# Performance work log

Measured on AMD Instinct MI355X. Metric: run time of the kernel, lower is better.

The kernel has to match this reference:

```python
import jax, jax.numpy as jnp
import numpy as np

# HEALPix face halo padding following the DLWP-HPX / HEALPixPad scheme:
# 12 faces (0-3 north polar, 4-7 equatorial, 8-11 south polar), each face
# padded with rotated/flipped slabs of its neighbor faces; missing tri-point
# corners of equatorial faces are synthesized from the two adjacent edges.

def _rot(f, k):
    # rotate a face [B, C, H, W] in its spatial plane
    return jnp.rot90(f, k, axes=(-2, -1))

def _corner_tl(top, left, p):
    # Missing top-left corner (tri-point): mean of the two adjacent pixels,
    # remaining halo pixels copied from the adjoining edges.
    ret = jnp.zeros(top.shape[:-2] + (p, p), top.dtype)
    ret = ret.at[..., -1, -1].set(0.5 * (top[..., -1, 0] + left[..., 0, -1]))
    for i in range(1, p):
        ret = ret.at[..., -i - 1, -1].set(top[..., -i - 1, 0])
        ret = ret.at[..., -1, -i - 1].set(left[..., 0, -i - 1])
    return ret

def _corner_br(bottom, right, p):
    # Missing bottom-right corner (tri-point)
    ret = jnp.zeros(bottom.shape[:-2] + (p, p), bottom.dtype)
    ret = ret.at[..., 0, 0].set(0.5 * (bottom[..., 0, -1] + right[..., -1, 0]))
    for i in range(1, p):
        ret = ret.at[..., i, 0].set(bottom[..., i, -1])
        ret = ret.at[..., 0, i].set(right[..., -1, i])
    return ret

def _assemble(c, t, tl, l, bl, b, br, r, tr, p):
    # c: [B,C,H,W]; neighbors already rotated into c's frame
    center = jnp.concatenate([t[..., -p:, :], c, b[..., :p, :]], axis=-2)
    left = jnp.concatenate([tl[..., -p:, -p:], l[..., :, -p:], bl[..., :p, -p:]], axis=-2)
    right = jnp.concatenate([tr[..., -p:, :p], r[..., :, :p], br[..., :p, :p]], axis=-2)
    return jnp.concatenate([left, center, right], axis=-1)  # [B,C,H+2p,W+2p]

def _healpix_pad(x, p):
    # x: [B, 12, C, H, W]
    f = [x[:, i] for i in range(12)]
    out = []
    # north polar faces 0-3: top-side neighbors must be rotated
    for i in range(4):
        out.append(_assemble(
            f[i], _rot(f[(i + 1) % 4], 1), _rot(f[(i + 2) % 4], 2),
            f[(i + 3) % 4], f[(i + 3) % 4], f[i + 4], f[i + 8],
            f[(i + 1) % 4 + 4], _rot(f[(i + 1) % 4], -1), p))
    # equatorial faces 4-7: no rotations; tl/br corners are tri-points
    for i in range(4):
        t, l = f[i], f[(i + 3) % 4]
        b, r = f[i + 8], f[(i + 1) % 4 + 4]
        out.append(_assemble(
            f[i + 4], t, _corner_tl(t, l, p), l, f[(i + 3) % 4 + 4],
            b, _corner_br(b, r, p), r, f[(i + 1) % 4], p))
    # south polar faces 8-11: bottom-side neighbors must be rotated
    for i in range(4):
        out.append(_assemble(
            f[i + 8], f[i + 4], f[i], f[(i + 3) % 4 + 4],
            _rot(f[(i + 3) % 4 + 8], -1), _rot(f[(i + 3) % 4 + 8], 1),
            _rot(f[(i + 3) % 4 + 8], 2), f[(i + 1) % 4 + 8], f[(i + 1) % 4 + 4], p))
    return jnp.stack(out, axis=1)  # [B, 12, C, H+2p, W+2p]


def setup_inputs() -> dict:
    key = jax.random.key(0)
    B, F, C, H = 2, 12, 64, 256
    x = jax.random.normal(key, (B, F, C, H, H), dtype=jnp.float32)
    return {"x": x, "pad": 1, "channels_last": False}


def reference(x, pad, channels_last):
    p = int(pad)
    if channels_last:
        x = jnp.moveaxis(x, -1, 2)  # (B,F,H,W,C) -> (B,F,C,H,W)
    if p == 0:
        out = x
    else:
        out = _healpix_pad(x, p)
    if channels_last:
        out = jnp.moveaxis(out, 2, -1)
    return out
```

## Files before the change

### kernel.cpp

```cpp
#include <hip/hip_runtime.h>


#define HH 256
#define HP 258
#define FACE_ELEMS (HH * HH)
#define OFACE_ELEMS (HP * HP)
#define NCH 64
#define HALO (2 * HP + 2 * HH)

__global__ void healpix_interior(const float* __restrict__ in,
                                 float* __restrict__ out, int total4) {
    int idx = blockIdx.x * blockDim.x + threadIdx.x;
    if (idx >= total4) return;
    int c4 = idx & 63;
    int t = idx >> 6;
    int r = t & 255;
    int pi = t >> 8;
    const float4 v = *reinterpret_cast<const float4*>(
        in + (size_t)pi * FACE_ELEMS + r * HH + (c4 << 2));
    float* o = out + (size_t)pi * OFACE_ELEMS + (size_t)(r + 1) * HP + (c4 << 2) + 1;
    o[0] = v.x; o[1] = v.y; o[2] = v.z; o[3] = v.w;
}

__global__ void healpix_halo(const float* __restrict__ in,
                             float* __restrict__ out, int totalh) {
    int idx = blockIdx.x * blockDim.x + threadIdx.x;
    if (idx >= totalh) return;
    int h = idx % HALO;
    int pi = idx / HALO;
    int face = (pi / NCH) % 12;

    int oy, ox;
    if (h < HP)           { oy = 0;      ox = h; }
    else if (h < 2 * HP)  { oy = HP - 1; ox = h - HP; }
    else if (h < 2 * HP + HH) { ox = 0;      oy = h - 2 * HP + 1; }
    else                      { ox = HP - 1; oy = h - 2 * HP - HH + 1; }

    const int i = face & 3;
    const int type = face >> 2;
    const bool top = (oy == 0), bot = (oy == HP - 1);
    const bool lft = (ox == 0), rgt = (ox == HP - 1);
    const int iy = oy - 1, ix = ox - 1;

    auto src = [&](int nf, int sy, int sx) -> float {
        return in[(size_t)(pi + (nf - face) * NCH) * FACE_ELEMS + sy * HH + sx];
    };

    float val;
    if (top && lft) {
        if (type == 0)      val = src((i + 2) & 3, 0, 0);
        else if (type == 1) val = 0.5f * (src(i, HH - 1, 0) +
                                          src((i + 3) & 3, 0, HH - 1));
        else                val = src(i, HH - 1, HH - 1);
    } else if (top && rgt) {
        if (type == 0)      val = src((i + 1) & 3, HH - 1, HH - 1);
        else if (type == 1) val = src((i + 1) & 3, HH - 1, 0);
        else                val = src(((i + 1) & 3) + 4, HH - 1, 0);
    } else if (bot && lft) {
        if (type == 0)      val = src((i + 3) & 3, 0, HH - 1);
        else if (type == 1) val = src(((i + 3) & 3) + 4, 0, HH - 1);
        else                val = src(((i + 3) & 3) + 8, 0, 0);
    } else if (bot && rgt) {
        if (type == 0)      val = src(i + 8, 0, 0);
        else if (type == 1) val = 0.5f * (src(i + 8, 0, HH - 1) +
                                          src(((i + 1) & 3) + 4, HH - 1, 0));
        else                val = src(((i + 3) & 3) + 8, HH - 1, HH - 1);
    } else if (top) {
        if (type == 0)      val = src((i + 1) & 3, ix, 0);
        else if (type == 1) val = src(i, HH - 1, ix);
        else                val = src(i + 4, HH - 1, ix);
    } else if (bot) {
        if (type == 0)      val = src(i + 4, 0, ix);
        else if (type == 1) val = src(i + 8, 0, ix);
        else                val = src(((i + 3) & 3) + 8, ix, HH - 1);
    } else if (lft) {
        if (type == 2)      val = src(((i + 3) & 3) + 4, iy, HH - 1);
        else                val = src((i + 3) & 3, iy, HH - 1);
    } else {
        if (type == 2)      val = src(((i + 1) & 3) + 8, iy, 0);
        else                val = src(((i + 1) & 3) + 4, iy, 0);
    }

    out[(size_t)pi * OFACE_ELEMS + (size_t)oy * HP + ox] = val;
}

extern "C" void kernel_launch(void* const* d_in, const int* in_sizes, int n_in,
                              void* d_out, int out_size, void* d_ws, size_t ws_size,
                              hipStream_t stream) {
    const float* x = (const float*)d_in[0];
    float* out = (float*)d_out;

    const int P = in_sizes[0] / FACE_ELEMS;

    const int total4 = P * HH * (HH / 4);
    const int blk = 256;
    healpix_interior<<<(total4 + blk - 1) / blk, blk, 0, stream>>>(x, out, total4);

    const int totalh = P * HALO;
    healpix_halo<<<(totalh + blk - 1) / blk, blk, 0, stream>>>(x, out, totalh);
}
```

Baseline: 708.5 us.

## Fuse interior and halo kernels into one LDS-staged row-band kernel

Replaces the separate interior-copy and halo kernels with one kernel. Each block stages 16 output rows, interior plus left and right halo columns, in shared memory, then writes them out as contiguous float4 stores. The goal is to remove the misaligned scalar stores of the interior kernel, since the output rows are offset by one, and the scattered halo writes of a second launch. It costs a shared-memory round trip and a barrier, and the top and bottom blocks have uneven work.

```diff
diff --git a/kernel.cpp b/kernel.cpp
--- a/kernel.cpp
+++ b/kernel.cpp
@@ -6,36 +6,9 @@
 #define FACE_ELEMS (HH * HH)
 #define OFACE_ELEMS (HP * HP)
 #define NCH 64
-#define HALO (2 * HP + 2 * HH)
 
-__global__ void healpix_interior(const float* __restrict__ in,
-                                 float* __restrict__ out, int total4) {
-    int idx = blockIdx.x * blockDim.x + threadIdx.x;
-    if (idx >= total4) return;
-    int c4 = idx & 63;
-    int t = idx >> 6;
-    int r = t & 255;
-    int pi = t >> 8;
-    const float4 v = *reinterpret_cast<const float4*>(
-        in + (size_t)pi * FACE_ELEMS + r * HH + (c4 << 2));
-    float* o = out + (size_t)pi * OFACE_ELEMS + (size_t)(r + 1) * HP + (c4 << 2) + 1;
-    o[0] = v.x; o[1] = v.y; o[2] = v.z; o[3] = v.w;
-}
-
-__global__ void healpix_halo(const float* __restrict__ in,
-                             float* __restrict__ out, int totalh) {
-    int idx = blockIdx.x * blockDim.x + threadIdx.x;
-    if (idx >= totalh) return;
-    int h = idx % HALO;
-    int pi = idx / HALO;
-    int face = (pi / NCH) % 12;
-
-    int oy, ox;
-    if (h < HP)           { oy = 0;      ox = h; }
-    else if (h < 2 * HP)  { oy = HP - 1; ox = h - HP; }
-    else if (h < 2 * HP + HH) { ox = 0;      oy = h - 2 * HP + 1; }
-    else                      { ox = HP - 1; oy = h - 2 * HP - HH + 1; }
-
+__device__ __forceinline__ float halo_val(const float* __restrict__ in,
+                                          int pi, int face, int oy, int ox) {
     const int i = face & 3;
     const int type = face >> 2;
     const bool top = (oy == 0), bot = (oy == HP - 1);
@@ -80,8 +53,64 @@
         if (type == 2)      val = src(((i + 1) & 3) + 8, iy, 0);
         else                val = src(((i + 1) & 3) + 4, iy, 0);
     }
+    return val;
+}
 
-    out[(size_t)pi * OFACE_ELEMS + (size_t)oy * HP + ox] = val;
+__global__ __launch_bounds__(256)
+void healpix_fused(const float* __restrict__ in, float* __restrict__ out) {
+    __shared__ __align__(16) float lds[16 * HP];
+
+    const int b  = blockIdx.x;
+    const int pi = blockIdx.y;
+    const int face = (pi / NCH) % 12;
+    const int t = threadIdx.x;
+
+    const float* inp = in + (size_t)pi * FACE_ELEMS;
+    const int oy0 = b * 16;
+
+    if (b >= 1 && b < 16) {
+        const int iy0 = oy0 - 1;
+        #pragma unroll
+        for (int k = 0; k < 16; ++k) {
+            const int f = t + 256 * k;
+            const int row = f >> 8, col = f & 255;
+            lds[row * HP + 1 + col] = inp[(iy0 + row) * HH + col];
+        }
+        if (t < 16)
+            lds[t * HP] = halo_val(in, pi, face, oy0 + t, 0);
+        else if (t < 32) {
+            const int r = t - 16;
+            lds[r * HP + HP - 1] = halo_val(in, pi, face, oy0 + r, HP - 1);
+        }
+    } else if (b == 0) {
+        for (int f = t; f < 15 * 256; f += 256) {
+            const int row = f >> 8, col = f & 255;
+            lds[(row + 1) * HP + 1 + col] = inp[row * HH + col];
+        }
+        for (int ox = t; ox < HP; ox += 256)
+            lds[ox] = halo_val(in, pi, face, 0, ox);
+        if (t >= 1 && t < 16)
+            lds[t * HP] = halo_val(in, pi, face, t, 0);
+        else if (t >= 17 && t < 32) {
+            const int r = t - 16;
+            lds[r * HP + HP - 1] = halo_val(in, pi, face, r, HP - 1);
+        }
+    } else {
+        if (t < 256) lds[1 + t] = inp[255 * HH + t];
+        if (t == 0) lds[0]      = halo_val(in, pi, face, 256, 0);
+        if (t == 1) lds[HP - 1] = halo_val(in, pi, face, 256, HP - 1);
+        for (int ox = t; ox < HP; ox += 256)
+            lds[HP + ox] = halo_val(in, pi, face, 257, ox);
+    }
+
+    __syncthreads();
+
+    const int n4 = (b < 16) ? (16 * HP / 4) : (2 * HP / 4);
+    float* outbase = out + (size_t)pi * OFACE_ELEMS + (size_t)oy0 * HP;
+    for (int q = t; q < n4; q += 256) {
+        const float4 v = *reinterpret_cast<const float4*>(&lds[4 * q]);
+        *reinterpret_cast<float4*>(&outbase[4 * q]) = v;
+    }
 }
 
 extern "C" void kernel_launch(void* const* d_in, const int* in_sizes, int n_in,
@@ -91,11 +120,6 @@
     float* out = (float*)d_out;
 
     const int P = in_sizes[0] / FACE_ELEMS;
-
-    const int total4 = P * HH * (HH / 4);
-    const int blk = 256;
-    healpix_interior<<<(total4 + blk - 1) / blk, blk, 0, stream>>>(x, out, total4);
-
-    const int totalh = P * HALO;
-    healpix_halo<<<(totalh + blk - 1) / blk, blk, 0, stream>>>(x, out, totalh);
+    dim3 grid(17, P);
+    healpix_fused<<<grid, 256, 0, stream>>>(x, out);
 }
```

Measured after the change: 655.9 us. 1.08x faster.
